# Optimization experiments

Hardware: AMD Instinct MI355X
Metric: run time of the kernel (lower is better)

Reference implementation:

```python
import jax, jax.numpy as jnp
import numpy as np
from jax import lax

N_NEURONS = 256
N_EDGES = 1024
BATCH = 128
HW = 28
KSIZE = 5
FC_HID = 200
N_CLS = 10


def _make_graph():
    # Replicates the torch __init__ random incidence construction; retries seeds
    # until the last neuron is reachable from neuron 0 (else torch forward loops forever).
    for seed in range(1000):
        rng = np.random.default_rng(seed)
        src = np.zeros(N_EDGES, np.int32)
        tgt = np.zeros(N_EDGES, np.int32)
        for e in range(N_EDGES):
            t = int(rng.choice(np.arange(1, N_NEURONS)))
            pool = np.arange(0, N_NEURONS - 1)
            if t < N_NEURONS - 1:
                pool = np.delete(pool, t)  # np.delete(range(0,N-1), target) as in source
            src[e] = int(rng.choice(pool))
            tgt[e] = t
        processed = np.zeros(N_NEURONS, bool)
        processed[0] = True
        frontier = [0]
        while frontier and not processed[-1]:
            nxt = set()
            for v in frontier:
                for m in tgt[src == v]:
                    if not processed[m]:
                        nxt.add(int(m))
            for m in nxt:
                processed[m] = True
            frontier = sorted(nxt)
        if processed[-1]:
            return src, tgt
    raise RuntimeError('no reachable graph found')


def _schedule(src, tgt, n):
    # Ordered input list per neuron (edge order, as np.where gives) + BFS waves from neuron 0.
    in_lists = [list(src[np.where(tgt == i)[0]]) for i in range(n)]
    waves = []
    processed = np.zeros(n, bool)
    frontier = [0]
    while True:
        waves.append(list(frontier))
        processed[frontier] = True
        if processed[n - 1]:
            break
        nxt = set()
        for v in frontier:
            for m in tgt[src == v]:
                if not processed[m]:
                    nxt.add(int(m))
        frontier = sorted(nxt)
        assert frontier, 'last neuron unreachable'
    return in_lists, waves


def setup_inputs() -> dict:
    src, tgt = _make_graph()
    rng = np.random.default_rng(123)
    deg = np.bincount(tgt, minlength=N_NEURONS)
    in_count = np.maximum(deg, 1)  # torch forces input_count>=1
    cmax = int(in_count.max())
    fan = np.sqrt(in_count.astype(np.float32) * KSIZE * KSIZE)
    conv_w = rng.normal(size=(N_NEURONS, 1, cmax, KSIZE, KSIZE)).astype(np.float32)
    conv_w /= fan[:, None, None, None, None]
    # zero out padding channels beyond each neuron's true in_count
    mask = (np.arange(cmax)[None, :] < in_count[:, None]).astype(np.float32)
    conv_w *= mask[:, None, :, None, None]
    conv_b = (0.01 * rng.normal(size=(N_NEURONS,))).astype(np.float32)
    deg_last = int(in_count[-1])
    fc1_w = (rng.normal(size=(FC_HID, deg_last * HW * HW)) / np.sqrt(deg_last * HW * HW)).astype(np.float32)
    fc1_b = np.zeros(FC_HID, np.float32)
    fc2_w = (rng.normal(size=(N_CLS, FC_HID)) / np.sqrt(FC_HID)).astype(np.float32)
    fc2_b = np.zeros(N_CLS, np.float32)
    x = jax.random.normal(jax.random.key(0), (BATCH, 1, HW, HW), jnp.float32)
    return {'x': x, 'src': jnp.asarray(src), 'tgt': jnp.asarray(tgt),
            'conv_w': jnp.asarray(conv_w), 'conv_b': jnp.asarray(conv_b),
            'fc1_w': jnp.asarray(fc1_w), 'fc1_b': jnp.asarray(fc1_b),
            'fc2_w': jnp.asarray(fc2_w), 'fc2_b': jnp.asarray(fc2_b)}


def _conv(g, w):  # g: [B,C,H,W], w: [1,C,5,5] -> [B,1,H,W], SAME padding 2
    return lax.conv_general_dilated(g, w, (1, 1), [(2, 2), (2, 2)])


def reference(x, src, tgt, conv_w, conv_b, fc1_w, fc1_b, fc2_w, fc2_b):
    src_np = np.asarray(src)
    tgt_np = np.asarray(tgt)
    n = int(conv_w.shape[0])
    cmax = int(conv_w.shape[2])
    B, H = x.shape[0], x.shape[2]
    in_lists, waves = _schedule(src_np, tgt_np, n)
    idx_pad = np.zeros((n, cmax), np.int32)  # pad idx 0 is safe: padded weight channels are zero
    for i, lst in enumerate(in_lists):
        idx_pad[i, :len(lst)] = lst

    out = jnp.zeros((n, B, H, H), x.dtype)  # per-neuron activations (unprocessed stay zero)
    hidden = None
    for wi, wave in enumerate(waves):
        snap = out  # within a wave, neurons read the previous wave's outputs
        if wi == 0:
            o0 = jax.nn.relu(_conv(x, conv_w[0, :, :1])[:, 0] + conv_b[0])
            out = out.at[0].set(o0)
            continue
        conv_nodes = [v for v in wave if v != n - 1]
        if conv_nodes:
            cn = jnp.asarray(np.array(conv_nodes, np.int32))
            g = snap[idx_pad[conv_nodes]]        # [K, Cmax, B, H, H]
            g = g.transpose(0, 2, 1, 3, 4)       # [K, B, Cmax, H, H]
            res = jax.vmap(_conv)(g, conv_w[cn])  # [K, B, 1, H, H]
            res = jax.nn.relu(res[:, :, 0] + conv_b[cn][:, None, None, None])
            out = out.at[cn].set(res)
        if (n - 1) in wave:
            lst = np.array(in_lists[n - 1], np.int32)
            comp = snap[lst].transpose(1, 0, 2, 3).reshape(B, -1)  # cat along channel then flatten
            hidden = jax.nn.relu(comp @ fc1_w.T + fc1_b)
    logits = hidden @ fc2_w.T + fc2_b
    return jax.nn.log_softmax(logits, axis=1)
```

## Files before the change

kernel.cpp:

```cpp
#include <hip/hip_runtime.h>

#define N_NEUR 256
#define N_EDGE 1024
#define BATCH  128
#define HWDIM  28
#define IMG    784
#define FCH    200
#define NCLS   10
#define INF_W  0x3fffffff
#define SLOTS  257
#define XSLOT  256
#define TSZ    1024
#define NT1    1024
#define NWAVE  16

#define ACT_FLOATS ((size_t)BATCH * SLOTS * TSZ)

__global__ __launch_bounds__(NT1, 4)
void conv_kernel(const float* __restrict__ x, const int* __restrict__ src,
                 const int* __restrict__ tgt, const float* __restrict__ conv_w,
                 const float* __restrict__ conv_b, float* __restrict__ act,
                 int* __restrict__ gsched, int cmax)
{
    const int tid = threadIdx.x;
    const int b   = blockIdx.x;

    __shared__ float s_tiles[NWAVE][2][TSZ];
    __shared__ int   s_off[N_NEUR + 2];
    __shared__ int   s_dat[N_EDGE];
    __shared__ int   s_wn[N_NEUR];
    __shared__ int   s_wo[N_NEUR + 2];
    __shared__ int   s_na[N_NEUR];
    __shared__ int   s_W;
    __shared__ int   s_done;

    int* e_src = (int*)&s_tiles[0][0][0];
    int* e_tgt = e_src + N_EDGE;
    int* wv    = e_tgt + N_EDGE;

    if (tid < N_EDGE) { e_src[tid] = src[tid]; e_tgt[tid] = tgt[tid]; }
    if (tid < N_NEUR) wv[tid] = (tid == 0) ? 0 : INF_W;
    __syncthreads();
    for (int w = 0; w < N_NEUR; ++w) {
        if (tid == 0) s_done = (wv[N_NEUR - 1] != INF_W);
        __syncthreads();
        if (s_done) break;
        {
            int s = e_src[tid], t = e_tgt[tid];
            if (wv[s] == w && wv[t] == INF_W) wv[t] = w + 1;
        }
        __syncthreads();
    }
    if (tid < N_NEUR) {
        int na = 0;
        const int wvv = wv[tid];
        for (int e = 0; e < N_EDGE; ++e)
            if (e_tgt[e] == tid && wv[e_src[e]] < wvv) ++na;
        if (tid == 0) na = 1;
        s_na[tid] = na;
    }
    __syncthreads();
    if (tid == 0) {
        int o = 0;
        for (int v = 0; v < N_NEUR; ++v) { s_off[v] = o; o += s_na[v]; }
        s_off[N_NEUR] = o;
        s_W = wv[N_NEUR - 1];
    }
    __syncthreads();
    if (tid < N_NEUR) {
        if (tid == 0) {
            s_dat[s_off[0]] = XSLOT;
        } else {
            int o = s_off[tid], c = 0;
            const int wvv = wv[tid];
            for (int e = 0; e < N_EDGE; ++e) {
                if (e_tgt[e] == tid) {
                    if (wv[e_src[e]] < wvv) s_dat[o++] = e_src[e] | (c << 9);
                    ++c;
                }
            }
        }
    }
    __syncthreads();
    {
        const int Wl = s_W;
        if (tid <= Wl + 1) {
            int cn = 0;
            for (int v2 = 0; v2 < N_NEUR - 1; ++v2) if (wv[v2] < tid) ++cn;
            s_wo[tid] = cn;
        }
        if (tid < N_NEUR - 1 && wv[tid] <= Wl) {
            int pos = 0; const int mw = wv[tid];
            for (int v2 = 0; v2 < N_NEUR - 1; ++v2) {
                int w2 = wv[v2];
                if (w2 < mw || (w2 == mw && v2 < tid)) ++pos;
            }
            s_wn[pos] = tid;
        }
    }
    __syncthreads();
    {
        const int naL = s_off[N_NEUR] - s_off[N_NEUR - 1];
        if (tid == 0) gsched[0] = naL;
        if (tid < naL) gsched[1 + tid] = s_dat[s_off[N_NEUR - 1] + tid];
    }
    for (int u = tid; u < SLOTS * 72; u += NT1) {
        const int t = u % 72, tile = u / 72;
        float* tp = act + (((size_t)b * SLOTS + tile) << 10);
        if (t < 16) {
            int eb = (t < 8) ? t * 8 : 960 + (t - 8) * 8;
            float4 z = make_float4(0.f, 0.f, 0.f, 0.f);
            ((float4*)(tp + eb))[0] = z; ((float4*)(tp + eb))[1] = z;
        } else {
            int s = t - 16;
            int eb = (2 + (s >> 1)) * 32 + ((s & 1) ? 30 : 0);
            *((float2*)(tp + eb)) = make_float2(0.f, 0.f);
        }
    }
    for (int u = tid; u < 196; u += NT1) {
        const int row = u / 7, col = (u - row * 7) * 4;
        float4 v4 = *(const float4*)(x + b * IMG + row * HWDIM + col);
        float* tp = act + (((size_t)b * SLOTS + XSLOT) << 10) + (row + 2) * 32 + col + 2;
        *(float2*)tp       = make_float2(v4.x, v4.y);
        *(float2*)(tp + 2) = make_float2(v4.z, v4.w);
    }
    __syncthreads();

    const int wid  = tid >> 6;
    const int lane = tid & 63;
    const bool la  = lane < 49;
    const int cy   = lane / 7, cx = lane - 7 * (lane / 7);
    float* bufA = &s_tiles[wid][0][0];
    float* bufB = &s_tiles[wid][1][0];

    auto loadStg = [&](float4* st, int oo) {
        const int uu = __builtin_amdgcn_readfirstlane(s_dat[oo]) & 511;
        const float4* gs = (const float4*)(act + (((size_t)b * SLOTS + uu) << 10));
        #pragma unroll
        for (int i = 0; i < 4; ++i) st[i] = gs[lane + 64 * i];
    };
    auto loadWg = [&](float* wg, int oo) {
        const int pk = __builtin_amdgcn_readfirstlane(s_dat[oo]);
        const int v2 = __builtin_amdgcn_readfirstlane(s_wn[0]);
        (void)v2;
        return pk;
    };
    (void)loadWg;
    auto storeLds = [&](float* buf, const float4* st) {
        float4* b4 = (float4*)buf;
        #pragma unroll
        for (int i = 0; i < 4; ++i) {
            const int fl = lane + 64 * i;
            const int lr = fl >> 3, cg = fl & 7;
            b4[(lr << 3) | (cg ^ ((lr >> 2) & 7))] = st[i];
        }
    };

    for (int w = 0; w <= s_W; ++w) {
        for (int ni = s_wo[w] + wid; ni < s_wo[w + 1]; ni += NWAVE) {
            const int v  = __builtin_amdgcn_readfirstlane(s_wn[ni]);
            const int o0 = s_off[v], o1 = s_off[v + 1];
            const float bias = conv_b[v];
            float acc[16];
            #pragma unroll
            for (int k = 0; k < 16; ++k) acc[k] = bias;

            float4 sA[4], sB[4];
            float  wA[25], wB[25];
            loadStg(sA, o0);
            {
                const int pk = __builtin_amdgcn_readfirstlane(s_dat[o0]);
                const float* wp = conv_w + ((size_t)v * cmax + (pk >> 9)) * 25;
                #pragma unroll
                for (int k = 0; k < 25; ++k) wA[k] = wp[k];
            }
            if (o0 + 1 < o1) {
                loadStg(sB, o0 + 1);
                const int pk = __builtin_amdgcn_readfirstlane(s_dat[o0 + 1]);
                const float* wp = conv_w + ((size_t)v * cmax + (pk >> 9)) * 25;
                #pragma unroll
                for (int k = 0; k < 25; ++k) wB[k] = wp[k];
            }

            auto computeBuf = [&](const float* buf, const float* wg) {
                if (!la) return;
                const float4* b4 = (const float4*)buf;
                #pragma unroll
                for (int r = 0; r < 8; ++r) {
                    const int row = 4 * cy + r;
                    const int sw  = (row >> 2) & 7;
                    float4 fa = b4[(row << 3) | (cx ^ sw)];
                    float4 fb = b4[(row << 3) | ((cx + 1) ^ sw)];
                    const float f[8] = {fa.x, fa.y, fa.z, fa.w, fb.x, fb.y, fb.z, fb.w};
                    #pragma unroll
                    for (int i = 0; i < 4; ++i) {
                        const int tr = r - i;
                        if (tr < 0 || tr > 4) continue;
                        #pragma unroll
                        for (int dx = 0; dx < 5; ++dx) {
                            const float wvv = wg[tr * 5 + dx];
                            #pragma unroll
                            for (int j = 0; j < 4; ++j)
                                acc[i * 4 + j] = fmaf(f[j + dx], wvv, acc[i * 4 + j]);
                        }
                    }
                }
            };

            int o = o0;
            while (true) {
                storeLds(bufA, sA);
                if (o + 2 < o1) loadStg(sA, o + 2);
                __builtin_amdgcn_sched_barrier(0);
                computeBuf(bufA, wA);
                if (o + 2 < o1) {
                    const int pk = __builtin_amdgcn_readfirstlane(s_dat[o + 2]);
                    const float* wp = conv_w + ((size_t)v * cmax + (pk >> 9)) * 25;
                    #pragma unroll
                    for (int k = 0; k < 25; ++k) wA[k] = wp[k];
                }
                ++o; if (o >= o1) break;
                storeLds(bufB, sB);
                if (o + 2 < o1) loadStg(sB, o + 2);
                __builtin_amdgcn_sched_barrier(0);
                computeBuf(bufB, wB);
                if (o + 2 < o1) {
                    const int pk = __builtin_amdgcn_readfirstlane(s_dat[o + 2]);
                    const float* wp = conv_w + ((size_t)v * cmax + (pk >> 9)) * 25;
                    #pragma unroll
                    for (int k = 0; k < 25; ++k) wB[k] = wp[k];
                }
                ++o; if (o >= o1) break;
            }

            if (la) {
                float* gd = act + (((size_t)b * SLOTS + v) << 10);
                #pragma unroll
                for (int i = 0; i < 4; ++i) {
                    float* p = gd + (2 + 4 * cy + i) * 32 + 2 + 4 * cx;
                    *(float2*)p       = make_float2(fmaxf(acc[i*4+0], 0.f), fmaxf(acc[i*4+1], 0.f));
                    *(float2*)(p + 2) = make_float2(fmaxf(acc[i*4+2], 0.f), fmaxf(acc[i*4+3], 0.f));
                }
            }
        }
        __syncthreads();
    }
}

#define FC1_BT 16
#define FC1_HT 16
#define FC1_STRIDE 900

__global__ __launch_bounds__(256, 2)
void fc1_kernel(const float* __restrict__ act, const float* __restrict__ fc1_w,
                const float* __restrict__ fc1_b, float* __restrict__ hidden,
                const int* __restrict__ gsched, int dlast)
{
    const int tid = threadIdx.x;
    const int bt  = blockIdx.x & 7;
    const int ht  = blockIdx.x >> 3;
    const int b0  = bt * FC1_BT;
    const int h0  = ht * FC1_HT;
    __shared__ float s_act[FC1_BT * FC1_STRIDE];
    const int naL = gsched[0];
    const int bb  = tid & 15, hh = tid >> 4;
    const int h   = h0 + hh;
    float acc = 0.f;

    for (int a = 0; a < naL; ++a) {
        const int pk = gsched[1 + a];
        const int u = pk & 511, k = pk >> 9;
        __syncthreads();
        for (int idx = tid; idx < FC1_BT * 224; idx += 256) {
            const int bi = idx / 224, rr = idx - bi * 224;
            const int r = rr >> 3, cg = rr & 7;
            const float4 vv = *((const float4*)(act +
                (((size_t)(b0 + bi) * SLOTS + u) << 10) + (r + 2) * 32) + cg);
            *(float4*)(&s_act[bi * FC1_STRIDE + r * 32 + cg * 4]) = vv;
        }
        __syncthreads();
        if (h < FCH) {
            const float* wrow = fc1_w + (size_t)h * ((size_t)dlast * IMG) + (size_t)k * IMG;
            const float* Tb   = &s_act[bb * FC1_STRIDE];
            for (int r = 0; r < HWDIM; ++r) {
                const float4* w4 = (const float4*)(wrow + r * HWDIM);
                const float*  tr = Tb + r * 32 + 2;
                #pragma unroll
                for (int q = 0; q < 7; ++q) {
                    const float4 wv = w4[q];
                    acc = fmaf(tr[4*q+0], wv.x, acc);
                    acc = fmaf(tr[4*q+1], wv.y, acc);
                    acc = fmaf(tr[4*q+2], wv.z, acc);
                    acc = fmaf(tr[4*q+3], wv.w, acc);
                }
            }
        }
    }
    if (h < FCH) hidden[(b0 + bb) * FCH + h] = fmaxf(acc + fc1_b[h], 0.f);
}

__global__ __launch_bounds__(128, 1)
void fc2_kernel(const float* __restrict__ hidden, const float* __restrict__ fc2_w,
                const float* __restrict__ fc2_b, float* __restrict__ dout)
{
    const int b = threadIdx.x;
    float hr[FCH];
    const float* hp = hidden + b * FCH;
    for (int h = 0; h < FCH; h += 2) {
        float2 v2 = *(const float2*)(hp + h);
        hr[h] = v2.x; hr[h + 1] = v2.y;
    }
    float lg[NCLS], m = -1e30f;
    #pragma unroll
    for (int c = 0; c < NCLS; ++c) {
        float a2 = fc2_b[c];
        const float* wr = fc2_w + c * FCH;
        for (int hh = 0; hh < FCH; ++hh) a2 = fmaf(hr[hh], wr[hh], a2);
        lg[c] = a2;
        m = fmaxf(m, a2);
    }
    float s = 0.0f;
    #pragma unroll
    for (int c = 0; c < NCLS; ++c) s += expf(lg[c] - m);
    const float ls = m + logf(s);
    #pragma unroll
    for (int c = 0; c < NCLS; ++c) dout[b * NCLS + c] = lg[c] - ls;
}

extern "C" void kernel_launch(void* const* d_in, const int* in_sizes, int n_in,
                              void* d_out, int out_size, void* d_ws, size_t ws_size,
                              hipStream_t stream) {
    const float* x      = (const float*)d_in[0];
    const int*   src    = (const int*)d_in[1];
    const int*   tgt    = (const int*)d_in[2];
    const float* conv_w = (const float*)d_in[3];
    const float* conv_b = (const float*)d_in[4];
    const float* fc1_w  = (const float*)d_in[5];
    const float* fc1_b  = (const float*)d_in[6];
    const float* fc2_w  = (const float*)d_in[7];
    const float* fc2_b  = (const float*)d_in[8];
    float* out = (float*)d_out;
    float* ws  = (float*)d_ws;

    const int cmax  = in_sizes[3] / (N_NEUR * 25);
    const int dlast = in_sizes[5] / (FCH * IMG);

    float* act    = ws;
    float* hidden = ws + ACT_FLOATS;
    int*   gsched = (int*)(hidden + BATCH * FCH);

    hipLaunchKernelGGL(conv_kernel, dim3(BATCH), dim3(NT1), 0, stream,
                       x, src, tgt, conv_w, conv_b, act, gsched, cmax);
    hipLaunchKernelGGL(fc1_kernel, dim3(104), dim3(256), 0, stream,
                       act, fc1_w, fc1_b, hidden, gsched, dlast);
    hipLaunchKernelGGL(fc2_kernel, dim3(1), dim3(128), 0, stream,
                       hidden, fc2_w, fc2_b, out);
}
```

Before: 349.3 us.

## Read conv input tiles directly from global memory instead of LDS staging

Removes the per-wave double-buffered LDS staging and software pipelining of input tiles. Each input channel is now read straight from global memory with per-lane float4 loads that feed the 5x5 FMA loop. This drops the LDS writes and reads and frees 128KB of shared memory, which may allow higher occupancy. In exchange it loses the explicit prefetch overlap and reads overlapping rows redundantly from global memory or cache.

```diff
diff --git a/kernel.cpp b/kernel.cpp
--- a/kernel.cpp
+++ b/kernel.cpp
@@ -25,37 +25,35 @@
     const int tid = threadIdx.x;
     const int b   = blockIdx.x;
 
-    __shared__ float s_tiles[NWAVE][2][TSZ];
-    __shared__ int   s_off[N_NEUR + 2];
-    __shared__ int   s_dat[N_EDGE];
-    __shared__ int   s_wn[N_NEUR];
-    __shared__ int   s_wo[N_NEUR + 2];
-    __shared__ int   s_na[N_NEUR];
-    __shared__ int   s_W;
-    __shared__ int   s_done;
-
-    int* e_src = (int*)&s_tiles[0][0][0];
-    int* e_tgt = e_src + N_EDGE;
-    int* wv    = e_tgt + N_EDGE;
+    __shared__ int e_src[N_EDGE];
+    __shared__ int e_tgt[N_EDGE];
+    __shared__ int wvs[N_NEUR];
+    __shared__ int s_off[N_NEUR + 2];
+    __shared__ int s_dat[N_EDGE];
+    __shared__ int s_wn[N_NEUR];
+    __shared__ int s_wo[N_NEUR + 2];
+    __shared__ int s_na[N_NEUR];
+    __shared__ int s_W;
+    __shared__ int s_done;
 
     if (tid < N_EDGE) { e_src[tid] = src[tid]; e_tgt[tid] = tgt[tid]; }
-    if (tid < N_NEUR) wv[tid] = (tid == 0) ? 0 : INF_W;
+    if (tid < N_NEUR) wvs[tid] = (tid == 0) ? 0 : INF_W;
     __syncthreads();
     for (int w = 0; w < N_NEUR; ++w) {
-        if (tid == 0) s_done = (wv[N_NEUR - 1] != INF_W);
+        if (tid == 0) s_done = (wvs[N_NEUR - 1] != INF_W);
         __syncthreads();
         if (s_done) break;
         {
             int s = e_src[tid], t = e_tgt[tid];
-            if (wv[s] == w && wv[t] == INF_W) wv[t] = w + 1;
+            if (wvs[s] == w && wvs[t] == INF_W) wvs[t] = w + 1;
         }
         __syncthreads();
     }
     if (tid < N_NEUR) {
         int na = 0;
-        const int wvv = wv[tid];
+        const int wvv = wvs[tid];
         for (int e = 0; e < N_EDGE; ++e)
-            if (e_tgt[e] == tid && wv[e_src[e]] < wvv) ++na;
+            if (e_tgt[e] == tid && wvs[e_src[e]] < wvv) ++na;
         if (tid == 0) na = 1;
         s_na[tid] = na;
     }
@@ -64,7 +62,7 @@
         int o = 0;
         for (int v = 0; v < N_NEUR; ++v) { s_off[v] = o; o += s_na[v]; }
         s_off[N_NEUR] = o;
-        s_W = wv[N_NEUR - 1];
+        s_W = wvs[N_NEUR - 1];
     }
     __syncthreads();
     if (tid < N_NEUR) {
@@ -72,10 +70,10 @@
             s_dat[s_off[0]] = XSLOT;
         } else {
             int o = s_off[tid], c = 0;
-            const int wvv = wv[tid];
+            const int wvv = wvs[tid];
             for (int e = 0; e < N_EDGE; ++e) {
                 if (e_tgt[e] == tid) {
-                    if (wv[e_src[e]] < wvv) s_dat[o++] = e_src[e] | (c << 9);
+                    if (wvs[e_src[e]] < wvv) s_dat[o++] = e_src[e] | (c << 9);
                     ++c;
                 }
             }
@@ -86,13 +84,13 @@
         const int Wl = s_W;
         if (tid <= Wl + 1) {
             int cn = 0;
-            for (int v2 = 0; v2 < N_NEUR - 1; ++v2) if (wv[v2] < tid) ++cn;
+            for (int v2 = 0; v2 < N_NEUR - 1; ++v2) if (wvs[v2] < tid) ++cn;
             s_wo[tid] = cn;
         }
-        if (tid < N_NEUR - 1 && wv[tid] <= Wl) {
-            int pos = 0; const int mw = wv[tid];
+        if (tid < N_NEUR - 1 && wvs[tid] <= Wl) {
+            int pos = 0; const int mw = wvs[tid];
             for (int v2 = 0; v2 < N_NEUR - 1; ++v2) {
-                int w2 = wv[v2];
+                int w2 = wvs[v2];
                 if (w2 < mw || (w2 == mw && v2 < tid)) ++pos;
             }
             s_wn[pos] = tid;
@@ -130,31 +128,6 @@
     const int lane = tid & 63;
     const bool la  = lane < 49;
     const int cy   = lane / 7, cx = lane - 7 * (lane / 7);
-    float* bufA = &s_tiles[wid][0][0];
-    float* bufB = &s_tiles[wid][1][0];
-
-    auto loadStg = [&](float4* st, int oo) {
-        const int uu = __builtin_amdgcn_readfirstlane(s_dat[oo]) & 511;
-        const float4* gs = (const float4*)(act + (((size_t)b * SLOTS + uu) << 10));
-        #pragma unroll
-        for (int i = 0; i < 4; ++i) st[i] = gs[lane + 64 * i];
-    };
-    auto loadWg = [&](float* wg, int oo) {
-        const int pk = __builtin_amdgcn_readfirstlane(s_dat[oo]);
-        const int v2 = __builtin_amdgcn_readfirstlane(s_wn[0]);
-        (void)v2;
-        return pk;
-    };
-    (void)loadWg;
-    auto storeLds = [&](float* buf, const float4* st) {
-        float4* b4 = (float4*)buf;
-        #pragma unroll
-        for (int i = 0; i < 4; ++i) {
-            const int fl = lane + 64 * i;
-            const int lr = fl >> 3, cg = fl & 7;
-            b4[(lr << 3) | (cg ^ ((lr >> 2) & 7))] = st[i];
-        }
-    };
 
     for (int w = 0; w <= s_W; ++w) {
         for (int ni = s_wo[w] + wid; ni < s_wo[w + 1]; ni += NWAVE) {
@@ -165,72 +138,41 @@
             #pragma unroll
             for (int k = 0; k < 16; ++k) acc[k] = bias;
 
-            float4 sA[4], sB[4];
-            float  wA[25], wB[25];
-            loadStg(sA, o0);
-            {
-                const int pk = __builtin_amdgcn_readfirstlane(s_dat[o0]);
-                const float* wp = conv_w + ((size_t)v * cmax + (pk >> 9)) * 25;
+            for (int o = o0; o < o1; ++o) {
+                const int pk = __builtin_amdgcn_readfirstlane(s_dat[o]);
+                const int u  = pk & 511;
+                const int c  = pk >> 9;
+                const float4* gs = (const float4*)(act + (((size_t)b * SLOTS + u) << 10));
+                const float*  wp = conv_w + ((size_t)v * cmax + c) * 25;
+                float wg[25];
                 #pragma unroll
-                for (int k = 0; k < 25; ++k) wA[k] = wp[k];
-            }
-            if (o0 + 1 < o1) {
-                loadStg(sB, o0 + 1);
-                const int pk = __builtin_amdgcn_readfirstlane(s_dat[o0 + 1]);
-                const float* wp = conv_w + ((size_t)v * cmax + (pk >> 9)) * 25;
-                #pragma unroll
-                for (int k = 0; k < 25; ++k) wB[k] = wp[k];
-            }
-
-            auto computeBuf = [&](const float* buf, const float* wg) {
-                if (!la) return;
-                const float4* b4 = (const float4*)buf;
-                #pragma unroll
-                for (int r = 0; r < 8; ++r) {
-                    const int row = 4 * cy + r;
-                    const int sw  = (row >> 2) & 7;
-                    float4 fa = b4[(row << 3) | (cx ^ sw)];
-                    float4 fb = b4[(row << 3) | ((cx + 1) ^ sw)];
-                    const float f[8] = {fa.x, fa.y, fa.z, fa.w, fb.x, fb.y, fb.z, fb.w};
+                for (int k = 0; k < 25; ++k) wg[k] = wp[k];
+                if (la) {
+                    float4 fa[8], fb[8];
                     #pragma unroll
-                    for (int i = 0; i < 4; ++i) {
-                        const int tr = r - i;
-                        if (tr < 0 || tr > 4) continue;
+                    for (int r = 0; r < 8; ++r) {
+                        const int ro = (4 * cy + r) * 8 + cx;
+                        fa[r] = gs[ro];
+                        fb[r] = gs[ro + 1];
+                    }
+                    #pragma unroll
+                    for (int r = 0; r < 8; ++r) {
+                        const float f[8] = {fa[r].x, fa[r].y, fa[r].z, fa[r].w,
+                                            fb[r].x, fb[r].y, fb[r].z, fb[r].w};
                         #pragma unroll
-                        for (int dx = 0; dx < 5; ++dx) {
-                            const float wvv = wg[tr * 5 + dx];
+                        for (int i = 0; i < 4; ++i) {
+                            const int tr = r - i;
+                            if (tr < 0 || tr > 4) continue;
                             #pragma unroll
-                            for (int j = 0; j < 4; ++j)
-                                acc[i * 4 + j] = fmaf(f[j + dx], wvv, acc[i * 4 + j]);
+                            for (int dx = 0; dx < 5; ++dx) {
+                                const float wvv = wg[tr * 5 + dx];
+                                #pragma unroll
+                                for (int j = 0; j < 4; ++j)
+                                    acc[i * 4 + j] = fmaf(f[j + dx], wvv, acc[i * 4 + j]);
+                            }
                         }
                     }
                 }
-            };
-
-            int o = o0;
-            while (true) {
-                storeLds(bufA, sA);
-                if (o + 2 < o1) loadStg(sA, o + 2);
-                __builtin_amdgcn_sched_barrier(0);
-                computeBuf(bufA, wA);
-                if (o + 2 < o1) {
-                    const int pk = __builtin_amdgcn_readfirstlane(s_dat[o + 2]);
-                    const float* wp = conv_w + ((size_t)v * cmax + (pk >> 9)) * 25;
-                    #pragma unroll
-                    for (int k = 0; k < 25; ++k) wA[k] = wp[k];
-                }
-                ++o; if (o >= o1) break;
-                storeLds(bufB, sB);
-                if (o + 2 < o1) loadStg(sB, o + 2);
-                __builtin_amdgcn_sched_barrier(0);
-                computeBuf(bufB, wB);
-                if (o + 2 < o1) {
-                    const int pk = __builtin_amdgcn_readfirstlane(s_dat[o + 2]);
-                    const float* wp = conv_w + ((size_t)v * cmax + (pk >> 9)) * 25;
-                    #pragma unroll
-                    for (int k = 0; k < 25; ++k) wB[k] = wp[k];
-                }
-                ++o; if (o >= o1) break;
             }
 
             if (la) {
```

Result: faster. 311.3 us (-10.9%).
